# Kernel optimization log

Hardware: AMD Instinct MI355X
Metric: run time of the kernel (lower is better)

## Reference

```python
import jax, jax.numpy as jnp
import numpy as np

D_MODEL = 1024
N_HEADS = 16


def get_freqs(seq, n_dim):
    # standard RoPE angles: (seq, n_dim//2)
    inv = 1.0 / (10000.0 ** (jnp.arange(0, n_dim, 2, dtype=jnp.float32) / n_dim))
    pos = jnp.arange(seq, dtype=jnp.float32)
    return pos[:, None] * inv[None, :]


def rope(x, freq):
    # x: (batch, seq, heads, n_dim); interleaved-pair rotation
    xf = x.astype(jnp.float32)
    x1 = xf[..., 0::2]
    x2 = xf[..., 1::2]
    cos = jnp.cos(freq)[None, :, None, :]  # (1, seq, 1, n_dim//2)
    sin = jnp.sin(freq)[None, :, None, :]
    r1 = x1 * cos - x2 * sin
    r2 = x1 * sin + x2 * cos
    out = jnp.stack([r1, r2], axis=-1).reshape(x.shape)
    return out.astype(x.dtype)


def setup_inputs() -> dict:
    key = jax.random.key(0)
    k1, k2, k3, k4, k5 = jax.random.split(key, 5)
    batch, seq = 2, 2048
    x = jax.random.normal(k1, (batch, seq, D_MODEL), dtype=jnp.float16)
    scale = jnp.float16(0.02)
    qw = jax.random.normal(k2, (D_MODEL, D_MODEL), dtype=jnp.float16) * scale
    kw = jax.random.normal(k3, (D_MODEL, D_MODEL), dtype=jnp.float16) * scale
    vw = jax.random.normal(k4, (D_MODEL, D_MODEL), dtype=jnp.float16) * scale
    ow = jax.random.normal(k5, (D_MODEL, D_MODEL), dtype=jnp.float16) * scale
    return {"x": x, "qw": qw, "kw": kw, "vw": vw, "ow": ow}


def reference(x, qw, kw, vw, ow):
    batch, seq, dim = x.shape
    n_heads = N_HEADS
    n_dim = dim // n_heads

    Q = (x @ qw).reshape(batch, seq, n_heads, n_dim)
    K = (x @ kw).reshape(batch, seq, n_heads, n_dim)
    V = (x @ vw).reshape(batch, seq, n_heads, n_dim)

    freq = get_freqs(seq, n_dim)
    Q = rope(Q, freq)
    K = rope(K, freq)

    Q = jnp.transpose(Q, (0, 2, 1, 3))  # (b, h, s, d)
    K = jnp.transpose(K, (0, 2, 1, 3))
    V = jnp.transpose(V, (0, 2, 1, 3))

    score = (Q @ jnp.swapaxes(K, -1, -2)) / jnp.sqrt(jnp.float16(dim))
    score = score.astype(jnp.float32)
    mask = jnp.tril(jnp.ones((1, 1, seq, seq), dtype=jnp.float32))
    score = score - 1e10 * (1.0 - mask)
    weights = jax.nn.softmax(score, axis=-1)  # fp32 (b, h, s, s)
    attn = weights @ V.astype(jnp.float32)

    merged = jnp.transpose(attn, (0, 2, 1, 3)).reshape(batch, seq, dim)
    out = merged @ ow.astype(jnp.float32)
    return out
```

## Files before the change

kernel.cpp:

```cpp
#include <hip/hip_runtime.h>
#include <math.h>

typedef _Float16 f16x8 __attribute__((ext_vector_type(8)));
typedef _Float16 f16x4 __attribute__((ext_vector_type(4)));
typedef float f32x4 __attribute__((ext_vector_type(4)));

#define SEQ 2048
#define DM 1024
#define NH 16
#define HD 64
#define MTOT 4096

#define NEG_BIG (-30000.0f)

__device__ __forceinline__ float ex2(float x) {
  return __builtin_amdgcn_exp2f(x);
}

__device__ __forceinline__ void gl_lds16(const _Float16* g, _Float16* l) {
  __builtin_amdgcn_global_load_lds(
      (const __attribute__((address_space(1))) unsigned int*)g,
      (__attribute__((address_space(3))) unsigned int*)l, 16, 0, 0);
}

__global__ __launch_bounds__(256) void prep(const float* __restrict__ x,
                                            const float* __restrict__ qw,
                                            const float* __restrict__ kw,
                                            const float* __restrict__ vw,
                                            const float* __restrict__ ow,
                                            _Float16* __restrict__ x16,
                                            _Float16* __restrict__ wT,
                                            float* __restrict__ tb) {
  const int z = blockIdx.z;
  const int t = threadIdx.x;
  if (z == 6) {
    const int idx = (blockIdx.y * 16 + blockIdx.x) * 256 + t;
    const int s = idx >> 5, d2 = idx & 31;
    const float inv = __powf(10000.0f, -(float)d2 * (1.0f / 32.0f));
    float c, sn;
    __sincosf((float)s * inv, &sn, &c);
    tb[2 * idx] = c;
    tb[2 * idx + 1] = sn;
    return;
  }
  if (z >= 4) {
    const int c = (z - 4) * 256 + blockIdx.y * 16 + blockIdx.x;
    const size_t base = (size_t)c * 8192;
#pragma unroll
    for (int rnd = 0; rnd < 4; ++rnd) {
      const size_t i = base + rnd * 2048 + t * 8;
      f32x4 a = *(const f32x4*)(x + i);
      f32x4 b = *(const f32x4*)(x + i + 4);
      f16x8 o;
#pragma unroll
      for (int j = 0; j < 4; ++j) { o[j] = (_Float16)a[j]; o[4 + j] = (_Float16)b[j]; }
      *(f16x8*)(x16 + i) = o;
    }
    return;
  }
  __shared__ float Ts[64][65];
  const float* srcs[4] = {qw, kw, vw, ow};
  const float* src = srcs[z];
  _Float16* dst = wT + (size_t)z * DM * DM;
  const int k0 = blockIdx.y * 64, n0 = blockIdx.x * 64;
  const int r = t >> 2, c4 = (t & 3) * 16;
  const float* sp = src + (size_t)(k0 + r) * DM + n0 + c4;
#pragma unroll
  for (int j = 0; j < 4; ++j) {
    f32x4 vv = *(const f32x4*)(sp + j * 4);
#pragma unroll
    for (int e = 0; e < 4; ++e) Ts[r][c4 + j * 4 + e] = vv[e];
  }
  __syncthreads();
  f16x8 o0, o1;
#pragma unroll
  for (int j = 0; j < 8; ++j) {
    o0[j] = (_Float16)Ts[c4 + j][r];
    o1[j] = (_Float16)Ts[c4 + 8 + j][r];
  }
  _Float16* dp = dst + (size_t)(n0 + r) * DM + k0 + c4;
  *(f16x8*)(dp) = o0;
  *(f16x8*)(dp + 8) = o1;
}

template <int BM, int BN, bool FUSED3, bool OUTF32, bool ROPE>
__global__ __launch_bounds__(256) void gemm_t(const _Float16* __restrict__ A,
                                              const _Float16* __restrict__ BT,
                                              void* __restrict__ Yv,
                                              const float* __restrict__ Tb,
                                              int M, int K) {
  constexpr int WM = BM / 2, WN = BN / 2;
  constexpr int MI = WM / 16, NI = WN / 16;
  __shared__ _Float16 As[BM * 32];
  __shared__ _Float16 Bs[BN * 32];
  const int tid = threadIdx.x;
  const int lane = tid & 63;
  const int fl = lane & 15, fh = lane >> 4;
  const int wave = tid >> 6;
  const int m0 = blockIdx.y * BM;
  int n0 = blockIdx.x * BN;
  int mat = 0;
  const _Float16* Bp = BT;
  char* Yp = (char*)Yv;
  if (FUSED3) {
    mat = n0 >> 10;
    n0 &= 1023;
    Bp = BT + (size_t)mat * DM * DM;
    Yp += (size_t)mat * M * DM * (OUTF32 ? 4 : 2);
  }
  const int wm = (wave >> 1) * WM, wn = (wave & 1) * WN;

  const int l4 = lane >> 2, lc = (lane & 3) * 8;

  f32x4 acc[MI][NI] = {};

  for (int k0 = 0; k0 < K; k0 += 32) {
    __syncthreads();
#pragma unroll
    for (int j = wave; j < BM / 16; j += 4)
      gl_lds16(A + (size_t)(m0 + j * 16 + l4) * K + k0 + lc, &As[j * 16 * 32]);
#pragma unroll
    for (int j = wave; j < BN / 16; j += 4)
      gl_lds16(Bp + (size_t)(n0 + j * 16 + l4) * K + k0 + lc, &Bs[j * 16 * 32]);
    __syncthreads();
    f16x8 af[MI], bf[NI];
#pragma unroll
    for (int mi = 0; mi < MI; ++mi)
      af[mi] = *(const f16x8*)(&As[(wm + mi * 16 + fl) * 32 + fh * 8]);
#pragma unroll
    for (int ni = 0; ni < NI; ++ni)
      bf[ni] = *(const f16x8*)(&Bs[(wn + ni * 16 + fl) * 32 + fh * 8]);
#pragma unroll
    for (int mi = 0; mi < MI; ++mi)
#pragma unroll
      for (int ni = 0; ni < NI; ++ni)
        acc[mi][ni] = __builtin_amdgcn_mfma_f32_16x16x32_f16(af[mi], bf[ni], acc[mi][ni], 0, 0, 0);
  }

#pragma unroll
  for (int mi = 0; mi < MI; ++mi)
#pragma unroll
    for (int ni = 0; ni < NI; ++ni) {
      const int gm = m0 + wm + mi * 16 + fh * 4;
      const int gn = n0 + wn + ni * 16 + fl;
      if (ROPE && mat < 2) {
        const int d2 = (gn & 63) >> 1;
        const float sgn = (gn & 1) ? 1.0f : -1.0f;
#pragma unroll
        for (int r = 0; r < 4; ++r) {
          const int s = (gm + r) & (SEQ - 1);
          const float2 cs = *(const float2*)(Tb + (size_t)((s << 5) + d2) * 2);
          const float v = acc[mi][ni][r];
          const float p = __shfl_xor(v, 1, 64);
          acc[mi][ni][r] = v * cs.x + sgn * p * cs.y;
        }
      }
#pragma unroll
      for (int r = 0; r < 4; ++r) {
        if (OUTF32)
          ((float*)Yp)[(size_t)(gm + r) * DM + gn] = acc[mi][ni][r];
        else
          ((_Float16*)Yp)[(size_t)(gm + r) * DM + gn] = (_Float16)acc[mi][ni][r];
      }
    }
}

__device__ __forceinline__ void qk_tile(const _Float16 (*Ks)[72],
                                        const f16x8 qf[2], f32x4 s[8],
                                        int fl, int fh) {
#pragma unroll
  for (int t = 0; t < 8; ++t) {
    f16x8 kf0 = *(const f16x8*)(&Ks[t * 16 + fl][fh * 8]);
    f16x8 kf1 = *(const f16x8*)(&Ks[t * 16 + fl][32 + fh * 8]);
    f32x4 z = {0.f, 0.f, 0.f, 0.f};
    z = __builtin_amdgcn_mfma_f32_16x16x32_f16(kf0, qf[0], z, 0, 0, 0);
    z = __builtin_amdgcn_mfma_f32_16x16x32_f16(kf1, qf[1], z, 0, 0, 0);
    s[t] = z;
  }
}

__device__ __forceinline__ void sm_pv(const _Float16 (*Vt)[136], f32x4 s[8],
                                      f32x4 o_acc[4], float& m_r, float& l_r,
                                      int kv0, int qg, bool do_mask, int fl,
                                      int fh) {
  if (do_mask) {
#pragma unroll
    for (int t = 0; t < 8; ++t)
#pragma unroll
      for (int r = 0; r < 4; ++r)
        if (kv0 + t * 16 + fh * 4 + r > qg) s[t][r] = NEG_BIG;
  }
  float mx = s[0][0];
#pragma unroll
  for (int t = 0; t < 8; ++t)
#pragma unroll
    for (int r = 0; r < 4; ++r) mx = fmaxf(mx, s[t][r]);
  mx = fmaxf(mx, __shfl_xor(mx, 16, 64));
  mx = fmaxf(mx, __shfl_xor(mx, 32, 64));
  float mn = m_r;
  if (__any(mx > m_r + 11.5f)) {
    mn = fmaxf(m_r, mx);
    const float a = ex2(m_r - mn);
    l_r *= a;
#pragma unroll
    for (int mt = 0; mt < 4; ++mt)
#pragma unroll
      for (int r = 0; r < 4; ++r) o_acc[mt][r] *= a;
    m_r = mn;
  }
  float rs = 0.f;
  f16x4 pb[8];
#pragma unroll
  for (int t = 0; t < 8; ++t) {
    float p0 = ex2(s[t][0] - mn);
    float p1 = ex2(s[t][1] - mn);
    float p2 = ex2(s[t][2] - mn);
    float p3 = ex2(s[t][3] - mn);
    rs += (p0 + p1) + (p2 + p3);
    f16x4 pk = {(_Float16)p0, (_Float16)p1, (_Float16)p2, (_Float16)p3};
    pb[t] = pk;
  }
  rs += __shfl_xor(rs, 16, 64);
  rs += __shfl_xor(rs, 32, 64);
  l_r += rs;
#pragma unroll
  for (int mt = 0; mt < 4; ++mt)
#pragma unroll
    for (int t = 0; t < 8; ++t) {
      f16x4 va = *(const f16x4*)(&Vt[mt * 16 + fl][t * 16 + fh * 4]);
      o_acc[mt] = __builtin_amdgcn_mfma_f32_16x16x16f16(va, pb[t], o_acc[mt], 0, 0, 0);
    }
}

__global__ __launch_bounds__(512, 2) void attn_kernel(const _Float16* __restrict__ Q,
                                                      const _Float16* __restrict__ K,
                                                      const _Float16* __restrict__ V,
                                                      _Float16* __restrict__ O) {
  __shared__ _Float16 Ks[128][72];
  __shared__ _Float16 Vt[64][136];

  const int tid = threadIdx.x;
  const int lane = tid & 63;
  const int fl = lane & 15, fh = lane >> 4;
  const int wave = tid >> 6;
  const int lin = blockIdx.y * 8 + blockIdx.x;
  const int w = (lin & 7) * 32 + (lin >> 3);
  const int p = w & 7;
  const int bh = w >> 3;
  const int b = bh >> 4, h = bh & 15;
  const int qt_lo = p * 128 + wave * 16;
  const int qt_hi = (15 - p) * 128 + wave * 16;

  const _Float16* Qb = Q + (size_t)b * SEQ * DM + h * HD;
  const _Float16* Kb = K + (size_t)b * SEQ * DM + h * HD;
  const _Float16* Vb = V + (size_t)b * SEQ * DM + h * HD;

  const _Float16 hs = (_Float16)(0.03125f * 1.44269504f);
  f16x8 qlo[2], qhi[2];
#pragma unroll
  for (int kh = 0; kh < 2; ++kh) {
    qlo[kh] = *(const f16x8*)(Qb + (size_t)(qt_lo + fl) * DM + kh * 32 + fh * 8);
    qhi[kh] = *(const f16x8*)(Qb + (size_t)(qt_hi + fl) * DM + kh * 32 + fh * 8);
#pragma unroll
    for (int j = 0; j < 8; ++j) { qlo[kh][j] *= hs; qhi[kh][j] *= hs; }
  }

  f32x4 o_lo[4] = {}, o_hi[4] = {};
  float m_lo = NEG_BIG, l_lo = 0.f, m_hi = NEG_BIG, l_hi = 0.f;

  const int sr = tid >> 3, e = tid & 7, sc8 = e * 8;
  const int cmax = 15 - p;

  f16x8 k0v = *(const f16x8*)(Kb + (size_t)(sr) * DM + sc8);
  f16x8 k1v = *(const f16x8*)(Kb + (size_t)(64 + sr) * DM + sc8);
  f16x8 v0v = *(const f16x8*)(Vb + (size_t)(sr) * DM + sc8);
  f16x8 v1v = *(const f16x8*)(Vb + (size_t)(64 + sr) * DM + sc8);

  for (int c = 0; c <= cmax; ++c) {
    const int kv0 = c * 128;
    __syncthreads();
    *(f16x8*)(&Ks[sr][sc8]) = k0v;
    *(f16x8*)(&Ks[64 + sr][sc8]) = k1v;
#pragma unroll
    for (int t = 0; t < 8; ++t) {
      const int jj = (t + e) & 7;
      Vt[sc8 + jj][sr] = v0v[jj];
      Vt[sc8 + jj][64 + sr] = v1v[jj];
    }
    __syncthreads();

    if (c < cmax) {
      const int kn = kv0 + 128;
      k0v = *(const f16x8*)(Kb + (size_t)(kn + sr) * DM + sc8);
      k1v = *(const f16x8*)(Kb + (size_t)(kn + 64 + sr) * DM + sc8);
      v0v = *(const f16x8*)(Vb + (size_t)(kn + sr) * DM + sc8);
      v1v = *(const f16x8*)(Vb + (size_t)(kn + 64 + sr) * DM + sc8);
    }

    if (c <= p) {
      f32x4 s_hi[8], s_lo[8];
      qk_tile(Ks, qhi, s_hi, fl, fh);
      qk_tile(Ks, qlo, s_lo, fl, fh);
      sm_pv(Vt, s_hi, o_hi, m_hi, l_hi, kv0, 0, false, fl, fh);
      sm_pv(Vt, s_lo, o_lo, m_lo, l_lo, kv0, qt_lo + fl, c == p, fl, fh);
    } else {
      f32x4 s_hi[8];
      qk_tile(Ks, qhi, s_hi, fl, fh);
      sm_pv(Vt, s_hi, o_hi, m_hi, l_hi, kv0, qt_hi + fl, c == cmax, fl, fh);
    }
  }

  {
    const float il = 1.0f / l_lo;
    _Float16* Op = O + ((size_t)b * SEQ + qt_lo + fl) * DM + h * HD;
#pragma unroll
    for (int mt = 0; mt < 4; ++mt) {
      f16x4 ov = {(_Float16)(o_lo[mt][0] * il), (_Float16)(o_lo[mt][1] * il),
                  (_Float16)(o_lo[mt][2] * il), (_Float16)(o_lo[mt][3] * il)};
      *(f16x4*)(Op + mt * 16 + fh * 4) = ov;
    }
  }
  {
    const float il = 1.0f / l_hi;
    _Float16* Op = O + ((size_t)b * SEQ + qt_hi + fl) * DM + h * HD;
#pragma unroll
    for (int mt = 0; mt < 4; ++mt) {
      f16x4 ov = {(_Float16)(o_hi[mt][0] * il), (_Float16)(o_hi[mt][1] * il),
                  (_Float16)(o_hi[mt][2] * il), (_Float16)(o_hi[mt][3] * il)};
      *(f16x4*)(Op + mt * 16 + fh * 4) = ov;
    }
  }
}

extern "C" void kernel_launch(void* const* d_in, const int* in_sizes, int n_in,
                              void* d_out, int out_size, void* d_ws, size_t ws_size,
                              hipStream_t stream) {
  const float* x = (const float*)d_in[0];
  const float* qw = (const float*)d_in[1];
  const float* kw = (const float*)d_in[2];
  const float* vw = (const float*)d_in[3];
  const float* ow = (const float*)d_in[4];
  float* out = (float*)d_out;

  const size_t MD = (size_t)MTOT * DM;
  _Float16* x16 = (_Float16*)d_ws;
  _Float16* wT = x16 + MD;
  _Float16* Qw = wT + 4 * (size_t)DM * DM;
  _Float16* Kw = Qw + MD;
  _Float16* Vw = Kw + MD;
  _Float16* Mw = x16;
  float* tb = out;

  prep<<<dim3(16, 16, 7), 256, 0, stream>>>(x, qw, kw, vw, ow, x16, wT, tb);

  gemm_t<128, 128, true, false, true><<<dim3(24, MTOT / 128), 256, 0, stream>>>(
      x16, wT, Qw, tb, MTOT, DM);

  attn_kernel<<<dim3(8, 32), 512, 0, stream>>>(Qw, Kw, Vw, Mw);

  gemm_t<64, 128, false, true, false><<<dim3(8, MTOT / 64), 256, 0, stream>>>(
      Mw, wT + 3 * (size_t)DM * DM, out, nullptr, MTOT, DM);
}
```

Before: 195.9 us.

## Split attention blocks into 256-thread halves and serialize hi/lo tile processing

The attention kernel moves from 512-thread blocks covering 128 query rows per pair to 256-thread blocks each covering 64 rows, doubling the grid to 512 blocks. Each block now loads the full 128-row K/V tile with four loads per thread instead of two. The hi and lo query tiles are processed one after another with a shared score buffer instead of both score sets live at once, which lowers register pressure. The aim is better occupancy and load balance across CUs, at the cost of loading each K/V tile twice as often in aggregate and more per-thread staging work.

```diff
diff --git a/kernel.cpp b/kernel.cpp
--- a/kernel.cpp
+++ b/kernel.cpp
@@ -232,7 +232,7 @@
     }
 }
 
-__global__ __launch_bounds__(512, 2) void attn_kernel(const _Float16* __restrict__ Q,
+__global__ __launch_bounds__(256, 2) void attn_kernel(const _Float16* __restrict__ Q,
                                                       const _Float16* __restrict__ K,
                                                       const _Float16* __restrict__ V,
                                                       _Float16* __restrict__ O) {
@@ -243,13 +243,15 @@
   const int lane = tid & 63;
   const int fl = lane & 15, fh = lane >> 4;
   const int wave = tid >> 6;
-  const int lin = blockIdx.y * 8 + blockIdx.x;
-  const int w = (lin & 7) * 32 + (lin >> 3);
-  const int p = w & 7;
-  const int bh = w >> 3;
+  const int lin = blockIdx.y * 16 + blockIdx.x;
+  const int w = (lin & 7) * 64 + (lin >> 3);
+  const int half = w & 1;
+  const int p = (w >> 1) & 7;
+  const int bh = w >> 4;
   const int b = bh >> 4, h = bh & 15;
-  const int qt_lo = p * 128 + wave * 16;
-  const int qt_hi = (15 - p) * 128 + wave * 16;
+  const int q0 = half * 64 + wave * 16;
+  const int qt_lo = p * 128 + q0;
+  const int qt_hi = (15 - p) * 128 + q0;
 
   const _Float16* Qb = Q + (size_t)b * SEQ * DM + h * HD;
   const _Float16* Kb = K + (size_t)b * SEQ * DM + h * HD;
@@ -271,42 +273,46 @@
   const int sr = tid >> 3, e = tid & 7, sc8 = e * 8;
   const int cmax = 15 - p;
 
-  f16x8 k0v = *(const f16x8*)(Kb + (size_t)(sr) * DM + sc8);
-  f16x8 k1v = *(const f16x8*)(Kb + (size_t)(64 + sr) * DM + sc8);
-  f16x8 v0v = *(const f16x8*)(Vb + (size_t)(sr) * DM + sc8);
-  f16x8 v1v = *(const f16x8*)(Vb + (size_t)(64 + sr) * DM + sc8);
+  f16x8 kv[4], vv[4];
+#pragma unroll
+  for (int i = 0; i < 4; ++i) {
+    kv[i] = *(const f16x8*)(Kb + (size_t)(i * 32 + sr) * DM + sc8);
+    vv[i] = *(const f16x8*)(Vb + (size_t)(i * 32 + sr) * DM + sc8);
+  }
 
   for (int c = 0; c <= cmax; ++c) {
     const int kv0 = c * 128;
     __syncthreads();
-    *(f16x8*)(&Ks[sr][sc8]) = k0v;
-    *(f16x8*)(&Ks[64 + sr][sc8]) = k1v;
-#pragma unroll
-    for (int t = 0; t < 8; ++t) {
-      const int jj = (t + e) & 7;
-      Vt[sc8 + jj][sr] = v0v[jj];
-      Vt[sc8 + jj][64 + sr] = v1v[jj];
-    }
+#pragma unroll
+    for (int i = 0; i < 4; ++i)
+      *(f16x8*)(&Ks[i * 32 + sr][sc8]) = kv[i];
+#pragma unroll
+    for (int i = 0; i < 4; ++i)
+#pragma unroll
+      for (int t = 0; t < 8; ++t) {
+        const int jj = (t + e) & 7;
+        Vt[sc8 + jj][i * 32 + sr] = vv[i][jj];
+      }
     __syncthreads();
 
     if (c < cmax) {
       const int kn = kv0 + 128;
-      k0v = *(const f16x8*)(Kb + (size_t)(kn + sr) * DM + sc8);
-      k1v = *(const f16x8*)(Kb + (size_t)(kn + 64 + sr) * DM + sc8);
-      v0v = *(const f16x8*)(Vb + (size_t)(kn + sr) * DM + sc8);
-      v1v = *(const f16x8*)(Vb + (size_t)(kn + 64 + sr) * DM + sc8);
-    }
-
+#pragma unroll
+      for (int i = 0; i < 4; ++i) {
+        kv[i] = *(const f16x8*)(Kb + (size_t)(kn + i * 32 + sr) * DM + sc8);
+        vv[i] = *(const f16x8*)(Vb + (size_t)(kn + i * 32 + sr) * DM + sc8);
+      }
+    }
+
+    {
+      f32x4 s[8];
+      qk_tile(Ks, qhi, s, fl, fh);
+      sm_pv(Vt, s, o_hi, m_hi, l_hi, kv0, qt_hi + fl, c == cmax, fl, fh);
+    }
     if (c <= p) {
-      f32x4 s_hi[8], s_lo[8];
-      qk_tile(Ks, qhi, s_hi, fl, fh);
-      qk_tile(Ks, qlo, s_lo, fl, fh);
-      sm_pv(Vt, s_hi, o_hi, m_hi, l_hi, kv0, 0, false, fl, fh);
-      sm_pv(Vt, s_lo, o_lo, m_lo, l_lo, kv0, qt_lo + fl, c == p, fl, fh);
-    } else {
-      f32x4 s_hi[8];
-      qk_tile(Ks, qhi, s_hi, fl, fh);
-      sm_pv(Vt, s_hi, o_hi, m_hi, l_hi, kv0, qt_hi + fl, c == cmax, fl, fh);
+      f32x4 s[8];
+      qk_tile(Ks, qlo, s, fl, fh);
+      sm_pv(Vt, s, o_lo, m_lo, l_lo, kv0, qt_lo + fl, c == p, fl, fh);
     }
   }
 
@@ -356,7 +362,7 @@
   gemm_t<128, 128, true, false, true><<<dim3(24, MTOT / 128), 256, 0, stream>>>(
       x16, wT, Qw, tb, MTOT, DM);
 
-  attn_kernel<<<dim3(8, 32), 512, 0, stream>>>(Qw, Kw, Vw, Mw);
+  attn_kernel<<<dim3(16, 32), 256, 0, stream>>>(Qw, Kw, Vw, Mw);
 
   gemm_t<64, 128, false, true, false><<<dim3(8, MTOT / 64), 256, 0, stream>>>(
       Mw, wT + 3 * (size_t)DM * DM, out, nullptr, MTOT, DM);
```

Result: slower. 207.9 us (+6.1%).
